# Kernel tuning notes

Measured on AMD Instinct MI355X. Metric: run time of the kernel, lower is better.

## Reference

```python
import jax, jax.numpy as jnp
import numpy as np


def _lstm_scan(xs, K, R, b, units):
    """Keras-style LSTM over time-major xs [T,B,F].
    Gate order i,f,g,o; recurrent_activation=sigmoid; activation=swish
    (applied to candidate g AND to cell state in h = o*swish(c))."""
    B = xs.shape[1]
    h0 = jnp.zeros((B, units), xs.dtype)
    c0 = jnp.zeros((B, units), xs.dtype)

    def step(carry, xt):
        h, c = carry
        z = xt @ K + h @ R + b  # [B, 4U]
        i, f, g, o = jnp.split(z, 4, axis=-1)
        i = jax.nn.sigmoid(i)
        f = jax.nn.sigmoid(f)
        g = jax.nn.swish(g)
        o = jax.nn.sigmoid(o)
        c = f * c + i * g
        h = o * jax.nn.swish(c)
        return (h, c), h

    _, hs = jax.lax.scan(step, (h0, c0), xs)
    return hs  # [T,B,U]


def setup_inputs() -> dict:
    B, T, F, U = 32, 512, 64, 512
    key = jax.random.key(0)
    ks = jax.random.split(key, 7)
    s = 0.05  # RandomUniform-ish small init scale
    x = jax.random.normal(ks[0], (B, T, F), jnp.float32)
    Kf = jax.random.uniform(ks[1], (F, 4 * U), jnp.float32, -s, s)
    Rf = jax.random.uniform(ks[2], (U, 4 * U), jnp.float32, -s, s)
    bf = jax.random.uniform(ks[3], (4 * U,), jnp.float32, -s, s)
    Kb = jax.random.uniform(ks[4], (F, 4 * U), jnp.float32, -s, s)
    Rb = jax.random.uniform(ks[5], (U, 4 * U), jnp.float32, -s, s)
    bb = jax.random.uniform(ks[6], (4 * U,), jnp.float32, -s, s)
    return {"x": x, "Kf": Kf, "Rf": Rf, "bf": bf, "Kb": Kb, "Rb": Rb, "bb": bb}


def reference(x, Kf, Rf, bf, Kb, Rb, bb):
    U = Rf.shape[0]
    xs = jnp.swapaxes(x, 0, 1)  # [T,B,F] time-major
    h_fwd = _lstm_scan(xs, Kf, Rf, bf, U)                      # [T,B,U]
    h_bwd = _lstm_scan(xs[::-1], Kb, Rb, bb, U)[::-1]          # [T,B,U]
    out = jnp.concatenate([h_fwd, h_bwd], axis=-1)             # [T,B,2U]
    return jnp.swapaxes(out, 0, 1)                              # [B,T,2U]
```

## Files before the change

### kernel.cpp

```cpp
#include <hip/hip_runtime.h>
#include <hip/hip_cooperative_groups.h>
#include <hip/hip_bf16.h>

namespace cg = cooperative_groups;

#define T_STEPS 512
#define BATCH   32
#define FDIM    64
#define UDIM    512
#define NWG_DIR 32
#define SENT    0xFFFFFFFFu

typedef __attribute__((ext_vector_type(8))) __bf16 bf16x8;
typedef __attribute__((ext_vector_type(4))) float  f32x4;


__global__ __launch_bounds__(512, 2)
void lstm_bidir_kernel(const float* __restrict__ x,
                       const float* __restrict__ Kf, const float* __restrict__ Rf,
                       const float* __restrict__ bfp,
                       const float* __restrict__ Kb, const float* __restrict__ Rb,
                       const float* __restrict__ bbp,
                       float* __restrict__ out, float* __restrict__ ws)
{
    __shared__ __align__(16) unsigned char hsb[BATCH * 1024];
    __shared__ __align__(16) unsigned char xsb[2][BATCH * 128];
    __shared__ __align__(16) float zbuf[BATCH * 68];
    __shared__ float cbuf[512];
    __shared__ float bsh[64];

    const int tid = threadIdx.x;
    const int wg  = blockIdx.x;
    const int dir   = wg >> 5;
    const int slice = wg & 31;
    const int colbase = slice * 16;

    const float* Kg = dir ? Kb : Kf;
    const float* Rg = dir ? Rb : Rf;
    const float* bg = dir ? bbp : bfp;

    unsigned char* wsb = (unsigned char*)ws;
    unsigned char* dirbase = wsb + (size_t)dir * 98304;

    {
        int g = wg * 512 + tid;
        ((unsigned int*)wsb)[g] = (((g >> 13) % 3) == 0) ? 0u : SENT;
        int g2 = g + 32768;
        if (g2 < 49152)
            ((unsigned int*)wsb)[g2] = (((g2 >> 13) % 3) == 0) ? 0u : SENT;
    }
    if (tid < 64) bsh[tid] = bg[(tid >> 4) * 512 + colbase + (tid & 15)];
    cbuf[tid] = 0.f;

    const int lane = tid & 63;
    const int w    = tid >> 6;
    const int mt   = w >> 2;
    const int gate = w & 3;
    const int bn   = lane & 15;
    const int kq   = lane >> 4;
    const int gcol = gate * 512 + colbase + bn;

    bf16x8 breg[18];
    #pragma unroll
    for (int s = 0; s < 16; ++s) {
        const int k0 = s * 32 + kq * 8;
        bf16x8 v;
        #pragma unroll
        for (int e = 0; e < 8; ++e)
            v[e] = (__bf16)Rg[(size_t)(k0 + e) * 2048 + gcol];
        breg[s] = v;
    }
    #pragma unroll
    for (int s = 0; s < 2; ++s) {
        const int k0 = s * 32 + kq * 8;
        bf16x8 v;
        #pragma unroll
        for (int e = 0; e < 8; ++e)
            v[e] = (__bf16)Kg[(size_t)(k0 + e) * 2048 + gcol];
        breg[16 + s] = v;
    }

    {
        const int t0 = dir ? (T_STEPS - 1) : 0;
        if (tid < 256) {
            int b = tid >> 3, m = tid & 7;
            const float4* xg = (const float4*)(x + (size_t)b * (T_STEPS * FDIM) + (size_t)t0 * FDIM + m * 8);
            float4 v0 = xg[0], v1 = xg[1];
            unsigned int p0 = ((unsigned int)__builtin_bit_cast(unsigned short, (__bf16)v0.x)) |
                              ((unsigned int)__builtin_bit_cast(unsigned short, (__bf16)v0.y) << 16);
            unsigned int p1 = ((unsigned int)__builtin_bit_cast(unsigned short, (__bf16)v0.z)) |
                              ((unsigned int)__builtin_bit_cast(unsigned short, (__bf16)v0.w) << 16);
            unsigned int p2 = ((unsigned int)__builtin_bit_cast(unsigned short, (__bf16)v1.x)) |
                              ((unsigned int)__builtin_bit_cast(unsigned short, (__bf16)v1.y) << 16);
            unsigned int p3 = ((unsigned int)__builtin_bit_cast(unsigned short, (__bf16)v1.z)) |
                              ((unsigned int)__builtin_bit_cast(unsigned short, (__bf16)v1.w) << 16);
            uint4 pk = make_uint4(p0, p1, p2, p3);
            *(uint4*)(xsb[0] + b * 128 + (m ^ (b & 7)) * 16) = pk;
        }
    }

    cg::grid_group grid = cg::this_grid();
    grid.sync();

    const int bb = tid >> 4;
    const int q  = tid & 15;
    float h_keep = 0.f;

    #pragma unroll 1
    for (int t = 0; t < T_STEPS; ++t) {
        if (t > 0) {
            const int txp = dir ? (T_STEPS - t) : (t - 1);
            out[(size_t)bb * (T_STEPS * 2 * UDIM) + (size_t)txp * (2 * UDIM)
                + dir * UDIM + colbase + q] = h_keep;
        }

        float4 xv0, xv1;
        const bool xload = (t + 1 < T_STEPS) && (tid < 256);
        const int bxr = tid >> 3, mx = tid & 7;
        if (xload) {
            const int tn = dir ? (T_STEPS - 2 - t) : (t + 1);
            const float4* xg = (const float4*)(x + (size_t)bxr * (T_STEPS * FDIM) + (size_t)tn * FDIM + mx * 8);
            xv0 = xg[0]; xv1 = xg[1];
        }

        uint4 r0, r1, r2, r3;
        {
            const unsigned char* srcrow = dirbase + (size_t)(t % 3) * 32768 + bb * 1024;
            for (;;) {
                asm volatile("global_load_dwordx4 %0, %1, off sc0 sc1"
                             : "=&v"(r0) : "v"(srcrow + (q +  0) * 16) : "memory");
                asm volatile("global_load_dwordx4 %0, %1, off sc0 sc1"
                             : "=&v"(r1) : "v"(srcrow + (q + 16) * 16) : "memory");
                asm volatile("global_load_dwordx4 %0, %1, off sc0 sc1"
                             : "=&v"(r2) : "v"(srcrow + (q + 32) * 16) : "memory");
                asm volatile("global_load_dwordx4 %0, %1, off sc0 sc1"
                             : "=&v"(r3) : "v"(srcrow + (q + 48) * 16) : "memory");
                asm volatile("s_waitcnt vmcnt(0)" ::: "memory");
                __builtin_amdgcn_sched_barrier(0);
                unsigned bad = (r0.x == SENT) | (r0.y == SENT) | (r0.z == SENT) | (r0.w == SENT)
                             | (r1.x == SENT) | (r1.y == SENT) | (r1.z == SENT) | (r1.w == SENT)
                             | (r2.x == SENT) | (r2.y == SENT) | (r2.z == SENT) | (r2.w == SENT)
                             | (r3.x == SENT) | (r3.y == SENT) | (r3.z == SENT) | (r3.w == SENT);
                if (!bad) break;
            }
        }

        if (tid < 256) {
            int prow = tid >> 3, pd = tid & 7;
            unsigned int* pp = (unsigned int*)(dirbase + (size_t)((t + 2) % 3) * 32768
                                               + prow * 1024 + colbase * 2) + pd;
            __hip_atomic_store(pp, SENT, __ATOMIC_RELAXED, __HIP_MEMORY_SCOPE_AGENT);
        }

        {
            const int inv = bb & 7;
            unsigned char* hrow = hsb + bb * 1024;
            *(uint4*)(hrow + (((q +  0) ^ inv) << 4)) = r0;
            *(uint4*)(hrow + (((q + 16) ^ inv) << 4)) = r1;
            *(uint4*)(hrow + (((q + 32) ^ inv) << 4)) = r2;
            *(uint4*)(hrow + (((q + 48) ^ inv) << 4)) = r3;
        }
        if (xload) {
            unsigned int p0 = ((unsigned int)__builtin_bit_cast(unsigned short, (__bf16)xv0.x)) |
                              ((unsigned int)__builtin_bit_cast(unsigned short, (__bf16)xv0.y) << 16);
            unsigned int p1 = ((unsigned int)__builtin_bit_cast(unsigned short, (__bf16)xv0.z)) |
                              ((unsigned int)__builtin_bit_cast(unsigned short, (__bf16)xv0.w) << 16);
            unsigned int p2 = ((unsigned int)__builtin_bit_cast(unsigned short, (__bf16)xv1.x)) |
                              ((unsigned int)__builtin_bit_cast(unsigned short, (__bf16)xv1.y) << 16);
            unsigned int p3 = ((unsigned int)__builtin_bit_cast(unsigned short, (__bf16)xv1.z)) |
                              ((unsigned int)__builtin_bit_cast(unsigned short, (__bf16)xv1.w) << 16);
            uint4 pk = make_uint4(p0, p1, p2, p3);
            *(uint4*)(xsb[(t + 1) & 1] + bxr * 128 + ((mx ^ (bxr & 7)) * 16)) = pk;
        }
        __syncthreads();

        f32x4 acc = {0.f, 0.f, 0.f, 0.f};
        {
            const int arow = mt * 16 + bn;
            const int inv  = arow & 7;
            const unsigned char* hrowA = hsb + arow * 1024;
            #pragma unroll
            for (int s = 0; s < 16; ++s) {
                int m = s * 4 + kq;
                bf16x8 a = *(const bf16x8*)(hrowA + ((m ^ inv) * 16));
                acc = __builtin_amdgcn_mfma_f32_16x16x32_bf16(a, breg[s], acc, 0, 0, 0);
            }
            const unsigned char* xrowA = xsb[t & 1] + arow * 128;
            #pragma unroll
            for (int s = 0; s < 2; ++s) {
                int m = s * 4 + kq;
                bf16x8 a = *(const bf16x8*)(xrowA + ((m ^ inv) * 16));
                acc = __builtin_amdgcn_mfma_f32_16x16x32_bf16(a, breg[16 + s], acc, 0, 0, 0);
            }
            const int zb = mt * 16 + kq * 4;
            #pragma unroll
            for (int j = 0; j < 4; ++j)
                zbuf[(zb + j) * 68 + gate * 16 + bn] = acc[j];
        }
        __syncthreads();

        {
            const float* zr = zbuf + bb * 68 + q;
            float zi = zr[0]  + bsh[q];
            float zf = zr[16] + bsh[16 + q];
            float zg = zr[32] + bsh[32 + q];
            float zo = zr[48] + bsh[48 + q];
            float gi = 1.f / (1.f + __expf(-zi));
            float gf = 1.f / (1.f + __expf(-zf));
            float gg = zg / (1.f + __expf(-zg));
            float go = 1.f / (1.f + __expf(-zo));
            float cv = gf * cbuf[tid] + gi * gg;
            cbuf[tid] = cv;
            float h  = go * (cv / (1.f + __expf(-cv)));
            h_keep = h;

            unsigned short hu = __builtin_bit_cast(unsigned short, (__bf16)h);
            int other = __shfl_xor((int)hu, 1);
            asm volatile("s_waitcnt vmcnt(0)" ::: "memory");
            if ((q & 1) == 0) {
                unsigned int packed = (unsigned int)hu | ((unsigned int)(unsigned short)other << 16);
                unsigned int* dst = (unsigned int*)(dirbase + (size_t)((t + 1) % 3) * 32768)
                                    + bb * 256 + ((colbase + q) >> 1);
                __hip_atomic_store(dst, packed, __ATOMIC_RELAXED, __HIP_MEMORY_SCOPE_AGENT);
            }
        }
    }

    {
        const int txl = dir ? 0 : (T_STEPS - 1);
        out[(size_t)bb * (T_STEPS * 2 * UDIM) + (size_t)txl * (2 * UDIM)
            + dir * UDIM + colbase + q] = h_keep;
    }
}

extern "C" void kernel_launch(void* const* d_in, const int* in_sizes, int n_in,
                              void* d_out, int out_size, void* d_ws, size_t ws_size,
                              hipStream_t stream) {
    (void)in_sizes; (void)n_in; (void)out_size; (void)ws_size;
    const float* x  = (const float*)d_in[0];
    const float* Kf = (const float*)d_in[1];
    const float* Rf = (const float*)d_in[2];
    const float* bf = (const float*)d_in[3];
    const float* Kb = (const float*)d_in[4];
    const float* Rb = (const float*)d_in[5];
    const float* bb = (const float*)d_in[6];
    float* out = (float*)d_out;
    float* ws  = (float*)d_ws;

    void* args[] = {&x, &Kf, &Rf, &bf, &Kb, &Rb, &bb, &out, &ws};
    hipLaunchCooperativeKernel((const void*)lstm_bidir_kernel,
                               dim3(64), dim3(512), args, 0, stream);
}
```

Before: 1.453 ms.

## Switch recurrent GEMM to 32x32x16 MFMA with split-K across waves

Replaces the per-step 16x16x32 MFMA tiling (each wave owns a 16-row by 16-column gate tile over the full K) with 32x32x16 MFMAs where each wave owns 32 columns and a quarter of K. Partial sums are written to a padded LDS buffer and reduced across the four K-slices before the gate math. This halves the per-wave dependent MFMA chain length and register B-fragments, at the cost of a larger LDS buffer and an extra reduction of 4 reads per gate. The output store of the previous step is also moved after the spin-wait on the h buffer.

```diff
diff --git a/kernel.cpp b/kernel.cpp
--- a/kernel.cpp
+++ b/kernel.cpp
@@ -11,8 +11,9 @@
 #define NWG_DIR 32
 #define SENT    0xFFFFFFFFu
 
-typedef __attribute__((ext_vector_type(8))) __bf16 bf16x8;
-typedef __attribute__((ext_vector_type(4))) float  f32x4;
+typedef __attribute__((ext_vector_type(8)))  __bf16 bf16x8;
+typedef __attribute__((ext_vector_type(4)))  float  f32x4;
+typedef __attribute__((ext_vector_type(16))) float  f32x16;
 
 
 __global__ __launch_bounds__(512, 2)
@@ -25,7 +26,7 @@
 {
     __shared__ __align__(16) unsigned char hsb[BATCH * 1024];
     __shared__ __align__(16) unsigned char xsb[2][BATCH * 128];
-    __shared__ __align__(16) float zbuf[BATCH * 68];
+    __shared__ __align__(16) float zbuf[8 * 32 * 33];
     __shared__ float cbuf[512];
     __shared__ float bsh[64];
 
@@ -54,30 +55,30 @@
 
     const int lane = tid & 63;
     const int w    = tid >> 6;
-    const int mt   = w >> 2;
-    const int gate = w & 3;
-    const int bn   = lane & 15;
-    const int kq   = lane >> 4;
-    const int gcol = gate * 512 + colbase + bn;
-
-    bf16x8 breg[18];
+    const int nt   = w >> 2;
+    const int kq   = w & 3;
+    const int lrow = lane & 31;
+    const int lhi  = lane >> 5;
+    const int c_local = nt * 32 + lrow;
+    const int gcol = (c_local >> 4) * 512 + colbase + (c_local & 15);
+
+    bf16x8 breg[9];
     #pragma unroll
-    for (int s = 0; s < 16; ++s) {
-        const int k0 = s * 32 + kq * 8;
+    for (int s = 0; s < 8; ++s) {
+        const int k0 = kq * 128 + s * 16 + lhi * 8;
         bf16x8 v;
         #pragma unroll
         for (int e = 0; e < 8; ++e)
             v[e] = (__bf16)Rg[(size_t)(k0 + e) * 2048 + gcol];
         breg[s] = v;
     }
-    #pragma unroll
-    for (int s = 0; s < 2; ++s) {
-        const int k0 = s * 32 + kq * 8;
+    {
+        const int k0 = kq * 16 + lhi * 8;
         bf16x8 v;
         #pragma unroll
         for (int e = 0; e < 8; ++e)
             v[e] = (__bf16)Kg[(size_t)(k0 + e) * 2048 + gcol];
-        breg[16 + s] = v;
+        breg[8] = v;
     }
 
     {
@@ -108,12 +109,6 @@
 
     #pragma unroll 1
     for (int t = 0; t < T_STEPS; ++t) {
-        if (t > 0) {
-            const int txp = dir ? (T_STEPS - t) : (t - 1);
-            out[(size_t)bb * (T_STEPS * 2 * UDIM) + (size_t)txp * (2 * UDIM)
-                + dir * UDIM + colbase + q] = h_keep;
-        }
-
         float4 xv0, xv1;
         const bool xload = (t + 1 < T_STEPS) && (tid < 256);
         const int bxr = tid >> 3, mx = tid & 7;
@@ -143,6 +138,12 @@
                              | (r3.x == SENT) | (r3.y == SENT) | (r3.z == SENT) | (r3.w == SENT);
                 if (!bad) break;
             }
+        }
+
+        if (t > 0) {
+            const int txp = dir ? (T_STEPS - t) : (t - 1);
+            out[(size_t)bb * (T_STEPS * 2 * UDIM) + (size_t)txp * (2 * UDIM)
+                + dir * UDIM + colbase + q] = h_keep;
         }
 
         if (tid < 256) {
@@ -174,41 +175,48 @@
         }
         __syncthreads();
 
-        f32x4 acc = {0.f, 0.f, 0.f, 0.f};
-        {
-            const int arow = mt * 16 + bn;
-            const int inv  = arow & 7;
-            const unsigned char* hrowA = hsb + arow * 1024;
+        {
+            f32x16 acc = {0.f,0.f,0.f,0.f,0.f,0.f,0.f,0.f,
+                          0.f,0.f,0.f,0.f,0.f,0.f,0.f,0.f};
+            const int inv = lrow & 7;
+            const unsigned char* hrowA = hsb + lrow * 1024;
             #pragma unroll
-            for (int s = 0; s < 16; ++s) {
-                int m = s * 4 + kq;
-                bf16x8 a = *(const bf16x8*)(hrowA + ((m ^ inv) * 16));
-                acc = __builtin_amdgcn_mfma_f32_16x16x32_bf16(a, breg[s], acc, 0, 0, 0);
-            }
-            const unsigned char* xrowA = xsb[t & 1] + arow * 128;
+            for (int s = 0; s < 8; ++s) {
+                int m = kq * 16 + s * 2 + lhi;
+                bf16x8 a = *(const bf16x8*)(hrowA + ((m ^ inv) << 4));
+                acc = __builtin_amdgcn_mfma_f32_32x32x16_bf16(a, breg[s], acc, 0, 0, 0);
+            }
+            {
+                const unsigned char* xrowA = xsb[t & 1] + lrow * 128;
+                int mxc = kq * 2 + lhi;
+                bf16x8 ax = *(const bf16x8*)(xrowA + ((mxc ^ inv) << 4));
+                acc = __builtin_amdgcn_mfma_f32_32x32x16_bf16(ax, breg[8], acc, 0, 0, 0);
+            }
             #pragma unroll
-            for (int s = 0; s < 2; ++s) {
-                int m = s * 4 + kq;
-                bf16x8 a = *(const bf16x8*)(xrowA + ((m ^ inv) * 16));
-                acc = __builtin_amdgcn_mfma_f32_16x16x32_bf16(a, breg[16 + s], acc, 0, 0, 0);
-            }
-            const int zb = mt * 16 + kq * 4;
+            for (int r = 0; r < 16; ++r) {
+                int row = (r & 3) + ((r >> 2) << 3) + (lhi << 2);
+                zbuf[(w * 32 + row) * 33 + lrow] = acc[r];
+            }
+        }
+        __syncthreads();
+
+        {
+            float zg4[4];
             #pragma unroll
-            for (int j = 0; j < 4; ++j)
-                zbuf[(zb + j) * 68 + gate * 16 + bn] = acc[j];
-        }
-        __syncthreads();
-
-        {
-            const float* zr = zbuf + bb * 68 + q;
-            float zi = zr[0]  + bsh[q];
-            float zf = zr[16] + bsh[16 + q];
-            float zg = zr[32] + bsh[32 + q];
-            float zo = zr[48] + bsh[48 + q];
-            float gi = 1.f / (1.f + __expf(-zi));
-            float gf = 1.f / (1.f + __expf(-zf));
-            float gg = zg / (1.f + __expf(-zg));
-            float go = 1.f / (1.f + __expf(-zo));
+            for (int g = 0; g < 4; ++g) {
+                const int cl  = g * 16 + q;
+                const int ntg = cl >> 5;
+                const int col = cl & 31;
+                float s = 0.f;
+                #pragma unroll
+                for (int k2 = 0; k2 < 4; ++k2)
+                    s += zbuf[((ntg * 4 + k2) * 32 + bb) * 33 + col];
+                zg4[g] = s + bsh[g * 16 + q];
+            }
+            float gi = 1.f / (1.f + __expf(-zg4[0]));
+            float gf = 1.f / (1.f + __expf(-zg4[1]));
+            float gg = zg4[2] / (1.f + __expf(-zg4[2]));
+            float go = 1.f / (1.f + __expf(-zg4[3]));
             float cv = gf * cbuf[tid] + gi * gg;
             cbuf[tid] = cv;
             float h  = go * (cv / (1.f + __expf(-cv)));
```

After: 1.456 ms. Within noise of the previous version (+0.2%).

## Split batch into two halves and pipeline h exchange with compute

Applied to the files above, without the earlier changes.

The per-step batch of 32 is split into two 16-row halves processed one after the other, so the cross-workgroup wait and load for one half's hidden state overlaps with the matmul and gate math of the other. The K dimension is also split across two wave groups, with partial sums reduced through shared memory, which halves the weight registers per thread. Launch bounds drop to one workgroup per CU. This adds more barriers per step and idles half the threads during the gate math. Correctness depends on the new sentinel reset ordering in the ring buffer.

```diff
diff --git a/kernel.cpp b/kernel.cpp
--- a/kernel.cpp
+++ b/kernel.cpp
@@ -5,17 +5,14 @@
 namespace cg = cooperative_groups;
 
 #define T_STEPS 512
-#define BATCH   32
-#define FDIM    64
 #define UDIM    512
-#define NWG_DIR 32
 #define SENT    0xFFFFFFFFu
 
 typedef __attribute__((ext_vector_type(8))) __bf16 bf16x8;
 typedef __attribute__((ext_vector_type(4))) float  f32x4;
 
 
-__global__ __launch_bounds__(512, 2)
+__global__ __launch_bounds__(512, 1)
 void lstm_bidir_kernel(const float* __restrict__ x,
                        const float* __restrict__ Kf, const float* __restrict__ Rf,
                        const float* __restrict__ bfp,
@@ -23,16 +20,17 @@
                        const float* __restrict__ bbp,
                        float* __restrict__ out, float* __restrict__ ws)
 {
-    __shared__ __align__(16) unsigned char hsb[BATCH * 1024];
-    __shared__ __align__(16) unsigned char xsb[2][BATCH * 128];
-    __shared__ __align__(16) float zbuf[BATCH * 68];
+    __shared__ __align__(16) unsigned char hAls[16 * 1024];
+    __shared__ __align__(16) unsigned char hBls[16 * 1024];
+    __shared__ __align__(16) unsigned char xls[32 * 128];
+    __shared__ __align__(16) float zA[32 * 68];
+    __shared__ __align__(16) float zB[32 * 68];
     __shared__ float cbuf[512];
     __shared__ float bsh[64];
 
     const int tid = threadIdx.x;
     const int wg  = blockIdx.x;
-    const int dir   = wg >> 5;
-    const int slice = wg & 31;
+    const int dir = wg >> 5, slice = wg & 31;
     const int colbase = slice * 16;
 
     const float* Kg = dir ? Kb : Kf;
@@ -54,113 +52,195 @@
 
     const int lane = tid & 63;
     const int w    = tid >> 6;
-    const int mt   = w >> 2;
     const int gate = w & 3;
+    const int kh   = w >> 2;
     const int bn   = lane & 15;
-    const int kq   = lane >> 4;
+    const int kg   = lane >> 4;
     const int gcol = gate * 512 + colbase + bn;
 
-    bf16x8 breg[18];
+    bf16x8 breg[9];
     #pragma unroll
-    for (int s = 0; s < 16; ++s) {
-        const int k0 = s * 32 + kq * 8;
+    for (int s = 0; s < 8; ++s) {
+        const int k0 = kh * 256 + s * 32 + kg * 8;
         bf16x8 v;
         #pragma unroll
-        for (int e = 0; e < 8; ++e)
-            v[e] = (__bf16)Rg[(size_t)(k0 + e) * 2048 + gcol];
+        for (int e = 0; e < 8; ++e) v[e] = (__bf16)Rg[(size_t)(k0 + e) * 2048 + gcol];
         breg[s] = v;
     }
-    #pragma unroll
-    for (int s = 0; s < 2; ++s) {
-        const int k0 = s * 32 + kq * 8;
+    {
+        const int k0 = kh * 32 + kg * 8;
         bf16x8 v;
         #pragma unroll
-        for (int e = 0; e < 8; ++e)
-            v[e] = (__bf16)Kg[(size_t)(k0 + e) * 2048 + gcol];
-        breg[16 + s] = v;
-    }
-
+        for (int e = 0; e < 8; ++e) v[e] = (__bf16)Kg[(size_t)(k0 + e) * 2048 + gcol];
+        breg[8] = v;
+    }
+
+    if (tid < 256) {
+        const int t0 = dir ? (T_STEPS - 1) : 0;
+        int b = tid >> 3, m = tid & 7;
+        const float4* xg = (const float4*)(x + (size_t)b * (T_STEPS * 64) + (size_t)t0 * 64 + m * 8);
+        float4 v0 = xg[0], v1 = xg[1];
+        unsigned int p0 = ((unsigned int)__builtin_bit_cast(unsigned short, (__bf16)v0.x)) |
+                          ((unsigned int)__builtin_bit_cast(unsigned short, (__bf16)v0.y) << 16);
+        unsigned int p1 = ((unsigned int)__builtin_bit_cast(unsigned short, (__bf16)v0.z)) |
+                          ((unsigned int)__builtin_bit_cast(unsigned short, (__bf16)v0.w) << 16);
+        unsigned int p2 = ((unsigned int)__builtin_bit_cast(unsigned short, (__bf16)v1.x)) |
+                          ((unsigned int)__builtin_bit_cast(unsigned short, (__bf16)v1.y) << 16);
+        unsigned int p3 = ((unsigned int)__builtin_bit_cast(unsigned short, (__bf16)v1.z)) |
+                          ((unsigned int)__builtin_bit_cast(unsigned short, (__bf16)v1.w) << 16);
+        *(uint4*)(xls + b * 128 + ((m ^ (b & 7)) << 4)) = make_uint4(p0, p1, p2, p3);
+    }
     {
-        const int t0 = dir ? (T_STEPS - 1) : 0;
-        if (tid < 256) {
-            int b = tid >> 3, m = tid & 7;
-            const float4* xg = (const float4*)(x + (size_t)b * (T_STEPS * FDIM) + (size_t)t0 * FDIM + m * 8);
-            float4 v0 = xg[0], v1 = xg[1];
-            unsigned int p0 = ((unsigned int)__builtin_bit_cast(unsigned short, (__bf16)v0.x)) |
-                              ((unsigned int)__builtin_bit_cast(unsigned short, (__bf16)v0.y) << 16);
-            unsigned int p1 = ((unsigned int)__builtin_bit_cast(unsigned short, (__bf16)v0.z)) |
-                              ((unsigned int)__builtin_bit_cast(unsigned short, (__bf16)v0.w) << 16);
-            unsigned int p2 = ((unsigned int)__builtin_bit_cast(unsigned short, (__bf16)v1.x)) |
-                              ((unsigned int)__builtin_bit_cast(unsigned short, (__bf16)v1.y) << 16);
-            unsigned int p3 = ((unsigned int)__builtin_bit_cast(unsigned short, (__bf16)v1.z)) |
-                              ((unsigned int)__builtin_bit_cast(unsigned short, (__bf16)v1.w) << 16);
-            uint4 pk = make_uint4(p0, p1, p2, p3);
-            *(uint4*)(xsb[0] + b * 128 + (m ^ (b & 7)) * 16) = pk;
-        }
+        uint4 z4 = make_uint4(0, 0, 0, 0);
+        *(uint4*)(hAls + tid * 32)      = z4;
+        *(uint4*)(hAls + tid * 32 + 16) = z4;
     }
 
     cg::grid_group grid = cg::this_grid();
     grid.sync();
 
-    const int bb = tid >> 4;
-    const int q  = tid & 15;
-    float h_keep = 0.f;
+    const int srow = tid >> 5;
+    const int sc   = tid & 31;
+    const int sinv = srow & 7;
+    const int gr   = tid >> 4;
+    const int gc   = tid & 15;
+
+    float h_keepA = 0.f, h_keepB = 0.f;
+    float4 xv0, xv1;
+    uint4 ra0, ra1, rb0, rb1;
+
+    {
+        const unsigned char* src = dirbase + (size_t)(16 + srow) * 1024;
+        asm volatile("global_load_dwordx4 %0, %1, off sc0 sc1" : "=&v"(rb0) : "v"(src + sc * 16) : "memory");
+        asm volatile("global_load_dwordx4 %0, %1, off sc0 sc1" : "=&v"(rb1) : "v"(src + (sc + 32) * 16) : "memory");
+    }
 
     #pragma unroll 1
     for (int t = 0; t < T_STEPS; ++t) {
-        if (t > 0) {
-            const int txp = dir ? (T_STEPS - t) : (t - 1);
-            out[(size_t)bb * (T_STEPS * 2 * UDIM) + (size_t)txp * (2 * UDIM)
-                + dir * UDIM + colbase + q] = h_keep;
-        }
-
-        float4 xv0, xv1;
-        const bool xload = (t + 1 < T_STEPS) && (tid < 256);
-        const int bxr = tid >> 3, mx = tid & 7;
-        if (xload) {
-            const int tn = dir ? (T_STEPS - 2 - t) : (t + 1);
-            const float4* xg = (const float4*)(x + (size_t)bxr * (T_STEPS * FDIM) + (size_t)tn * FDIM + mx * 8);
-            xv0 = xg[0]; xv1 = xg[1];
-        }
-
-        uint4 r0, r1, r2, r3;
+        __syncthreads();
+
         {
-            const unsigned char* srcrow = dirbase + (size_t)(t % 3) * 32768 + bb * 1024;
-            for (;;) {
-                asm volatile("global_load_dwordx4 %0, %1, off sc0 sc1"
-                             : "=&v"(r0) : "v"(srcrow + (q +  0) * 16) : "memory");
-                asm volatile("global_load_dwordx4 %0, %1, off sc0 sc1"
-                             : "=&v"(r1) : "v"(srcrow + (q + 16) * 16) : "memory");
-                asm volatile("global_load_dwordx4 %0, %1, off sc0 sc1"
-                             : "=&v"(r2) : "v"(srcrow + (q + 32) * 16) : "memory");
-                asm volatile("global_load_dwordx4 %0, %1, off sc0 sc1"
-                             : "=&v"(r3) : "v"(srcrow + (q + 48) * 16) : "memory");
+            const int r = lane & 15, inv = r & 7;
+            f32x4 a0 = {0.f,0.f,0.f,0.f}, a1 = {0.f,0.f,0.f,0.f};
+            #pragma unroll
+            for (int s = 0; s < 8; ++s) {
+                int ch = kh * 32 + s * 4 + kg;
+                bf16x8 a = *(const bf16x8*)(hAls + r * 1024 + ((ch ^ inv) << 4));
+                if (s & 1) a1 = __builtin_amdgcn_mfma_f32_16x16x32_bf16(a, breg[s], a1, 0, 0, 0);
+                else       a0 = __builtin_amdgcn_mfma_f32_16x16x32_bf16(a, breg[s], a0, 0, 0, 0);
+            }
+            {
+                int chx = kh * 4 + kg;
+                bf16x8 ax = *(const bf16x8*)(xls + r * 128 + ((chx ^ inv) << 4));
+                a0 = __builtin_amdgcn_mfma_f32_16x16x32_bf16(ax, breg[8], a0, 0, 0, 0);
+            }
+            #pragma unroll
+            for (int j = 0; j < 4; ++j)
+                zA[(kh * 16 + kg * 4 + j) * 68 + gate * 16 + bn] = a0[j] + a1[j];
+        }
+        __syncthreads();
+
+        if (tid < 256) {
+            float zi = zA[gr * 68 +      gc] + zA[(16 + gr) * 68 +      gc] + bsh[gc];
+            float zf = zA[gr * 68 + 16 + gc] + zA[(16 + gr) * 68 + 16 + gc] + bsh[16 + gc];
+            float zg = zA[gr * 68 + 32 + gc] + zA[(16 + gr) * 68 + 32 + gc] + bsh[32 + gc];
+            float zo = zA[gr * 68 + 48 + gc] + zA[(16 + gr) * 68 + 48 + gc] + bsh[48 + gc];
+            float gi = 1.f / (1.f + __expf(-zi));
+            float gf = 1.f / (1.f + __expf(-zf));
+            float gg = zg / (1.f + __expf(-zg));
+            float go = 1.f / (1.f + __expf(-zo));
+            float cv = gf * cbuf[tid] + gi * gg;
+            cbuf[tid] = cv;
+            h_keepA = go * (cv / (1.f + __expf(-cv)));
+        }
+
+        asm volatile("s_waitcnt vmcnt(0)" ::: "memory");
+        __builtin_amdgcn_sched_barrier(0);
+        {
+            const unsigned char* src = dirbase + (size_t)(t % 3) * 32768 + (size_t)(16 + srow) * 1024;
+            unsigned bad = (rb0.x == SENT) | (rb0.y == SENT) | (rb0.z == SENT) | (rb0.w == SENT)
+                         | (rb1.x == SENT) | (rb1.y == SENT) | (rb1.z == SENT) | (rb1.w == SENT);
+            while (bad) {
+                asm volatile("global_load_dwordx4 %0, %1, off sc0 sc1" : "=&v"(rb0) : "v"(src + sc * 16) : "memory");
+                asm volatile("global_load_dwordx4 %0, %1, off sc0 sc1" : "=&v"(rb1) : "v"(src + (sc + 32) * 16) : "memory");
                 asm volatile("s_waitcnt vmcnt(0)" ::: "memory");
                 __builtin_amdgcn_sched_barrier(0);
-                unsigned bad = (r0.x == SENT) | (r0.y == SENT) | (r0.z == SENT) | (r0.w == SENT)
-                             | (r1.x == SENT) | (r1.y == SENT) | (r1.z == SENT) | (r1.w == SENT)
-                             | (r2.x == SENT) | (r2.y == SENT) | (r2.z == SENT) | (r2.w == SENT)
-                             | (r3.x == SENT) | (r3.y == SENT) | (r3.z == SENT) | (r3.w == SENT);
-                if (!bad) break;
+                bad = (rb0.x == SENT) | (rb0.y == SENT) | (rb0.z == SENT) | (rb0.w == SENT)
+                    | (rb1.x == SENT) | (rb1.y == SENT) | (rb1.z == SENT) | (rb1.w == SENT);
             }
         }
 
         if (tid < 256) {
-            int prow = tid >> 3, pd = tid & 7;
-            unsigned int* pp = (unsigned int*)(dirbase + (size_t)((t + 2) % 3) * 32768
-                                               + prow * 1024 + colbase * 2) + pd;
-            __hip_atomic_store(pp, SENT, __ATOMIC_RELAXED, __HIP_MEMORY_SCOPE_AGENT);
-        }
+            unsigned short hu = __builtin_bit_cast(unsigned short, (__bf16)h_keepA);
+            int other = __shfl_xor((int)hu, 1);
+            if ((gc & 1) == 0) {
+                unsigned int packed = (unsigned int)hu | ((unsigned int)(unsigned short)other << 16);
+                unsigned int* dst = (unsigned int*)(dirbase + (size_t)((t + 1) % 3) * 32768)
+                                    + gr * 256 + ((colbase + gc) >> 1);
+                __hip_atomic_store(dst, packed, __ATOMIC_RELAXED, __HIP_MEMORY_SCOPE_AGENT);
+            }
+        }
+
+        *(uint4*)(hBls + srow * 1024 + ((sc        ^ sinv) << 4)) = rb0;
+        *(uint4*)(hBls + srow * 1024 + (((sc + 32) ^ sinv) << 4)) = rb1;
+
+        if (t > 0 && tid < 256) {
+            int txp = dir ? (T_STEPS - t) : (t - 1);
+            out[(size_t)(16 + gr) * (T_STEPS * 2 * UDIM) + (size_t)txp * (2 * UDIM)
+                + dir * UDIM + colbase + gc] = h_keepB;
+        }
+
+        if (t + 1 < T_STEPS) {
+            const unsigned char* src = dirbase + (size_t)((t + 1) % 3) * 32768 + (size_t)srow * 1024;
+            asm volatile("global_load_dwordx4 %0, %1, off sc0 sc1" : "=&v"(ra0) : "v"(src + sc * 16) : "memory");
+            asm volatile("global_load_dwordx4 %0, %1, off sc0 sc1" : "=&v"(ra1) : "v"(src + (sc + 32) * 16) : "memory");
+            if (tid < 256) {
+                const int tn = dir ? (T_STEPS - 2 - t) : (t + 1);
+                int b = tid >> 3, m = tid & 7;
+                const float4* xg = (const float4*)(x + (size_t)b * (T_STEPS * 64) + (size_t)tn * 64 + m * 8);
+                xv0 = xg[0]; xv1 = xg[1];
+            }
+        }
+
+        __syncthreads();
 
         {
-            const int inv = bb & 7;
-            unsigned char* hrow = hsb + bb * 1024;
-            *(uint4*)(hrow + (((q +  0) ^ inv) << 4)) = r0;
-            *(uint4*)(hrow + (((q + 16) ^ inv) << 4)) = r1;
-            *(uint4*)(hrow + (((q + 32) ^ inv) << 4)) = r2;
-            *(uint4*)(hrow + (((q + 48) ^ inv) << 4)) = r3;
-        }
-        if (xload) {
+            const int r = lane & 15, inv = r & 7;
+            f32x4 a0 = {0.f,0.f,0.f,0.f}, a1 = {0.f,0.f,0.f,0.f};
+            #pragma unroll
+            for (int s = 0; s < 8; ++s) {
+                int ch = kh * 32 + s * 4 + kg;
+                bf16x8 a = *(const bf16x8*)(hBls + r * 1024 + ((ch ^ inv) << 4));
+                if (s & 1) a1 = __builtin_amdgcn_mfma_f32_16x16x32_bf16(a, breg[s], a1, 0, 0, 0);
+                else       a0 = __builtin_amdgcn_mfma_f32_16x16x32_bf16(a, breg[s], a0, 0, 0, 0);
+            }
+            {
+                int chx = kh * 4 + kg;
+                int xr = 16 + r;
+                bf16x8 ax = *(const bf16x8*)(xls + xr * 128 + ((chx ^ inv) << 4));
+                a0 = __builtin_amdgcn_mfma_f32_16x16x32_bf16(ax, breg[8], a0, 0, 0, 0);
+            }
+            #pragma unroll
+            for (int j = 0; j < 4; ++j)
+                zB[(kh * 16 + kg * 4 + j) * 68 + gate * 16 + bn] = a0[j] + a1[j];
+        }
+        __syncthreads();
+
+        if (tid < 256) {
+            float zi = zB[gr * 68 +      gc] + zB[(16 + gr) * 68 +      gc] + bsh[gc];
+            float zf = zB[gr * 68 + 16 + gc] + zB[(16 + gr) * 68 + 16 + gc] + bsh[16 + gc];
+            float zg = zB[gr * 68 + 32 + gc] + zB[(16 + gr) * 68 + 32 + gc] + bsh[32 + gc];
+            float zo = zB[gr * 68 + 48 + gc] + zB[(16 + gr) * 68 + 48 + gc] + bsh[48 + gc];
+            float gi = 1.f / (1.f + __expf(-zi));
+            float gf = 1.f / (1.f + __expf(-zf));
+            float gg = zg / (1.f + __expf(-zg));
+            float go = 1.f / (1.f + __expf(-zo));
+            float cv = gf * cbuf[256 + tid] + gi * gg;
+            cbuf[256 + tid] = cv;
+            h_keepB = go * (cv / (1.f + __expf(-cv)));
+        }
+        if (t + 1 < T_STEPS && tid < 256) {
+            int b = tid >> 3, m = tid & 7;
             unsigned int p0 = ((unsigned int)__builtin_bit_cast(unsigned short, (__bf16)xv0.x)) |
                               ((unsigned int)__builtin_bit_cast(unsigned short, (__bf16)xv0.y) << 16);
             unsigned int p1 = ((unsigned int)__builtin_bit_cast(unsigned short, (__bf16)xv0.z)) |
@@ -169,67 +249,62 @@
                               ((unsigned int)__builtin_bit_cast(unsigned short, (__bf16)xv1.y) << 16);
             unsigned int p3 = ((unsigned int)__builtin_bit_cast(unsigned short, (__bf16)xv1.z)) |
                               ((unsigned int)__builtin_bit_cast(unsigned short, (__bf16)xv1.w) << 16);
-            uint4 pk = make_uint4(p0, p1, p2, p3);
-            *(uint4*)(xsb[(t + 1) & 1] + bxr * 128 + ((mx ^ (bxr & 7)) * 16)) = pk;
-        }
-        __syncthreads();
-
-        f32x4 acc = {0.f, 0.f, 0.f, 0.f};
-        {
-            const int arow = mt * 16 + bn;
-            const int inv  = arow & 7;
-            const unsigned char* hrowA = hsb + arow * 1024;
-            #pragma unroll
-            for (int s = 0; s < 16; ++s) {
-                int m = s * 4 + kq;
-                bf16x8 a = *(const bf16x8*)(hrowA + ((m ^ inv) * 16));
-                acc = __builtin_amdgcn_mfma_f32_16x16x32_bf16(a, breg[s], acc, 0, 0, 0);
-            }
-            const unsigned char* xrowA = xsb[t & 1] + arow * 128;
-            #pragma unroll
-            for (int s = 0; s < 2; ++s) {
-                int m = s * 4 + kq;
-                bf16x8 a = *(const bf16x8*)(xrowA + ((m ^ inv) * 16));
-                acc = __builtin_amdgcn_mfma_f32_16x16x32_bf16(a, breg[16 + s], acc, 0, 0, 0);
-            }
-            const int zb = mt * 16 + kq * 4;
-            #pragma unroll
-            for (int j = 0; j < 4; ++j)
-                zbuf[(zb + j) * 68 + gate * 16 + bn] = acc[j];
-        }
-        __syncthreads();
-
-        {
-            const float* zr = zbuf + bb * 68 + q;
-            float zi = zr[0]  + bsh[q];
-            float zf = zr[16] + bsh[16 + q];
-            float zg = zr[32] + bsh[32 + q];
-            float zo = zr[48] + bsh[48 + q];
-            float gi = 1.f / (1.f + __expf(-zi));
-            float gf = 1.f / (1.f + __expf(-zf));
-            float gg = zg / (1.f + __expf(-zg));
-            float go = 1.f / (1.f + __expf(-zo));
-            float cv = gf * cbuf[tid] + gi * gg;
-            cbuf[tid] = cv;
-            float h  = go * (cv / (1.f + __expf(-cv)));
-            h_keep = h;
-
-            unsigned short hu = __builtin_bit_cast(unsigned short, (__bf16)h);
-            int other = __shfl_xor((int)hu, 1);
+            *(uint4*)(xls + b * 128 + ((m ^ (b & 7)) << 4)) = make_uint4(p0, p1, p2, p3);
+        }
+
+        if (t + 1 < T_STEPS) {
             asm volatile("s_waitcnt vmcnt(0)" ::: "memory");
-            if ((q & 1) == 0) {
-                unsigned int packed = (unsigned int)hu | ((unsigned int)(unsigned short)other << 16);
-                unsigned int* dst = (unsigned int*)(dirbase + (size_t)((t + 1) % 3) * 32768)
-                                    + bb * 256 + ((colbase + q) >> 1);
-                __hip_atomic_store(dst, packed, __ATOMIC_RELAXED, __HIP_MEMORY_SCOPE_AGENT);
-            }
-        }
-    }
-
-    {
-        const int txl = dir ? 0 : (T_STEPS - 1);
-        out[(size_t)bb * (T_STEPS * 2 * UDIM) + (size_t)txl * (2 * UDIM)
-            + dir * UDIM + colbase + q] = h_keep;
+            __builtin_amdgcn_sched_barrier(0);
+            {
+                const unsigned char* src = dirbase + (size_t)((t + 1) % 3) * 32768 + (size_t)srow * 1024;
+                unsigned bad = (ra0.x == SENT) | (ra0.y == SENT) | (ra0.z == SENT) | (ra0.w == SENT)
+                             | (ra1.x == SENT) | (ra1.y == SENT) | (ra1.z == SENT) | (ra1.w == SENT);
+                while (bad) {
+                    asm volatile("global_load_dwordx4 %0, %1, off sc0 sc1" : "=&v"(ra0) : "v"(src + sc * 16) : "memory");
+                    asm volatile("global_load_dwordx4 %0, %1, off sc0 sc1" : "=&v"(ra1) : "v"(src + (sc + 32) * 16) : "memory");
+                    asm volatile("s_waitcnt vmcnt(0)" ::: "memory");
+                    __builtin_amdgcn_sched_barrier(0);
+                    bad = (ra0.x == SENT) | (ra0.y == SENT) | (ra0.z == SENT) | (ra0.w == SENT)
+                        | (ra1.x == SENT) | (ra1.y == SENT) | (ra1.z == SENT) | (ra1.w == SENT);
+                }
+            }
+            if (tid < 256) {
+                unsigned short hu = __builtin_bit_cast(unsigned short, (__bf16)h_keepB);
+                int other = __shfl_xor((int)hu, 1);
+                if ((gc & 1) == 0) {
+                    unsigned int packed = (unsigned int)hu | ((unsigned int)(unsigned short)other << 16);
+                    unsigned int* dst = (unsigned int*)(dirbase + (size_t)((t + 1) % 3) * 32768)
+                                        + (16 + gr) * 256 + ((colbase + gc) >> 1);
+                    __hip_atomic_store(dst, packed, __ATOMIC_RELAXED, __HIP_MEMORY_SCOPE_AGENT);
+                }
+            }
+            *(uint4*)(hAls + srow * 1024 + ((sc        ^ sinv) << 4)) = ra0;
+            *(uint4*)(hAls + srow * 1024 + (((sc + 32) ^ sinv) << 4)) = ra1;
+            if (tid < 256) {
+                int prow = tid >> 3, dw = tid & 7;
+                unsigned int* pp = (unsigned int*)(dirbase + (size_t)(t % 3) * 32768
+                                                   + prow * 1024 + colbase * 2) + dw;
+                __hip_atomic_store(pp, SENT, __ATOMIC_RELAXED, __HIP_MEMORY_SCOPE_AGENT);
+            }
+            if (tid < 256) {
+                int tx = dir ? (T_STEPS - 1 - t) : t;
+                out[(size_t)gr * (T_STEPS * 2 * UDIM) + (size_t)tx * (2 * UDIM)
+                    + dir * UDIM + colbase + gc] = h_keepA;
+            }
+            {
+                const unsigned char* src = dirbase + (size_t)((t + 1) % 3) * 32768 + (size_t)(16 + srow) * 1024;
+                asm volatile("global_load_dwordx4 %0, %1, off sc0 sc1" : "=&v"(rb0) : "v"(src + sc * 16) : "memory");
+                asm volatile("global_load_dwordx4 %0, %1, off sc0 sc1" : "=&v"(rb1) : "v"(src + (sc + 32) * 16) : "memory");
+            }
+        }
+    }
+
+    if (tid < 256) {
+        int tx = dir ? 0 : (T_STEPS - 1);
+        out[(size_t)gr * (T_STEPS * 2 * UDIM) + (size_t)tx * (2 * UDIM)
+            + dir * UDIM + colbase + gc] = h_keepA;
+        out[(size_t)(16 + gr) * (T_STEPS * 2 * UDIM) + (size_t)tx * (2 * UDIM)
+            + dir * UDIM + colbase + gc] = h_keepB;
     }
 }
 
```

Measured after the change: 2.287 ms. 57.4% more time.
